# Kernel optimization log

Measured on AMD Instinct MI355X. Metric: run time of the kernel, lower is better.

The kernel has to match this reference:

```python
import jax, jax.numpy as jnp
import numpy as np

EPS_IN = 1e-4   # added to concatenated inputs before variance (as in original)
EPS_OUT = 1e-6  # added after NaN masking (as in original)


def _mdl_masked(a, b):
    """Diagonal-covariance Mahalanobis distance matrix [B,B], NaN-masked, +eps.

    Original TF code builds diag(var), inverts it with tf.linalg.inv and does two
    dense matmuls; mathematically that is an elementwise divide by the per-feature
    variance followed by diff @ diff^T, which is what we compute here.
    """
    in_co = jnp.concatenate((a, b), axis=0) + EPS_IN          # [2B, D]
    var = jnp.var(in_co, axis=0)                              # [D] per-feature variance
    diff = a - b                                              # [B, D]
    q = jnp.einsum('id,jd->ij', diff / var, diff)             # [B, B] = diff @ inv(diag(var)) @ diff^T
    # sqrt of negative entries is NaN in the original; multiply_no_nan zeroes them.
    neg = q < 0.0
    mdist = jnp.where(neg, 0.0, jnp.sqrt(jnp.where(neg, 1.0, q)))
    return mdist + EPS_OUT


def setup_inputs() -> dict:
    key = jax.random.key(0)
    k1, k2, k3 = jax.random.split(key, 3)
    B, D = 8192, 64
    return {
        'anchor': jax.random.normal(k1, (B, D), dtype=jnp.float32),
        'positive': jax.random.normal(k2, (B, D), dtype=jnp.float32),
        'negative': jax.random.normal(k3, (B, D), dtype=jnp.float32),
    }


def reference(anchor, positive, negative):
    ap = _mdl_masked(anchor, positive)   # [B, B]
    an = _mdl_masked(anchor, negative)   # [B, B]
    ap_dis = jnp.sum(ap, axis=-1)        # [B]
    ap_neg = jnp.sum(an, axis=-1)        # [B]
    return (ap_dis, ap_neg)
```

## Files before the change

kernel.cpp:

```cpp
#include <hip/hip_runtime.h>
#include <hip/hip_bf16.h>


typedef short bf16x8 __attribute__((ext_vector_type(8)));
typedef unsigned short u16x8 __attribute__((ext_vector_type(8)));
typedef float f32x4 __attribute__((ext_vector_type(4)));

#define BROWS 8192
#define DFEAT 64
#define NCO   16384
#define EPS_IN  1e-4f
#define EPS_OUT 1e-6f

#define WS_EHL_F 512
#define EHL_PAIR_USHORTS ((size_t)BROWS * 128)

static __device__ inline unsigned short f2bf_rne(float x) {
  unsigned u = __float_as_uint(x);
  unsigned r = (u + 0x7FFF + ((u >> 16) & 1)) >> 16;
  return (unsigned short)r;
}
static __device__ inline float bf2f(unsigned short s) {
  return __uint_as_float(((unsigned)s) << 16);
}

__global__ __launch_bounds__(256) void stats_kernel(
    const float* __restrict__ a, const float* __restrict__ p,
    const float* __restrict__ n, float* __restrict__ stats) {
  __shared__ float acc[6][64];
  int tid = threadIdx.x;
  for (int v = tid; v < 384; v += 256) acc[v >> 6][v & 63] = 0.f;
  __syncthreads();
  const float4* A4 = (const float4*)a;
  const float4* P4 = (const float4*)p;
  const float4* N4 = (const float4*)n;
  size_t base = (size_t)blockIdx.x * 512 + tid;
  float s[3][4] = {}, q[3][4] = {};
  #pragma unroll
  for (int k = 0; k < 2; ++k) {
    size_t idx = base + k * 256;
    float4 va = A4[idx], vp = P4[idx], vn = N4[idx];
    float ea[4] = {va.x, va.y, va.z, va.w};
    float ep[4] = {vp.x, vp.y, vp.z, vp.w};
    float en[4] = {vn.x, vn.y, vn.z, vn.w};
    #pragma unroll
    for (int f = 0; f < 4; ++f) {
      float x0 = ea[f] + EPS_IN; s[0][f] += x0; q[0][f] += x0 * x0;
      float x1 = ep[f] + EPS_IN; s[1][f] += x1; q[1][f] += x1 * x1;
      float x2 = en[f] + EPS_IN; s[2][f] += x2; q[2][f] += x2 * x2;
    }
  }
  #pragma unroll
  for (int g = 0; g < 3; ++g)
    #pragma unroll
    for (int f = 0; f < 4; ++f) {
      float vs = s[g][f], vq = q[g][f];
      vs += __shfl_xor(vs, 16); vs += __shfl_xor(vs, 32);
      vq += __shfl_xor(vq, 16); vq += __shfl_xor(vq, 32);
      s[g][f] = vs; q[g][f] = vq;
    }
  int lane = tid & 63;
  if (lane < 16) {
    int d0 = lane * 4;
    #pragma unroll
    for (int g = 0; g < 3; ++g)
      #pragma unroll
      for (int f = 0; f < 4; ++f) {
        atomicAdd(&acc[2 * g][d0 + f], s[g][f]);
        atomicAdd(&acc[2 * g + 1][d0 + f], q[g][f]);
      }
  }
  __syncthreads();
  for (int v = tid; v < 384; v += 256)
    atomicAdd(&stats[v], acc[v >> 6][v & 63]);
}

__global__ __launch_bounds__(256) void prep_kernel(
    const float* __restrict__ a, const float* __restrict__ p,
    const float* __restrict__ n, const float* __restrict__ stats,
    unsigned short* __restrict__ EHL, float* __restrict__ out) {
  __shared__ float is_s[64];
  int pair = blockIdx.x >> 8;
  int tb   = blockIdx.x & 255;
  int tid  = threadIdx.x;
  if (tid < 32) out[blockIdx.x * 32 + tid] = 8192.0f * EPS_OUT;
  if (tid < 64) {
    float sa = stats[tid], qa = stats[64 + tid];
    float sb = pair ? stats[256 + tid] : stats[128 + tid];
    float qb = pair ? stats[320 + tid] : stats[192 + tid];
    const float invN = 1.0f / (float)NCO;
    float m = (sa + sb) * invN;
    float v = (qa + qb) * invN - m * m;
    is_s[tid] = 1.0f / sqrtf(v);
  }
  __syncthreads();
  const float* bptr = pair ? n : p;
  unsigned short* dst = EHL + (size_t)pair * EHL_PAIR_USHORTS;
  int c0 = tid & 7;
  int rl = tid >> 3;
  int row = tb * 32 + rl;
  int d0 = c0 * 8;
  const float* ar = a    + (size_t)row * DFEAT + d0;
  const float* br = bptr + (size_t)row * DFEAT + d0;
  float4 a0 = *(const float4*)(ar);
  float4 a1 = *(const float4*)(ar + 4);
  float4 b0 = *(const float4*)(br);
  float4 b1 = *(const float4*)(br + 4);
  float e[8] = {a0.x - b0.x, a0.y - b0.y, a0.z - b0.z, a0.w - b0.w,
                a1.x - b1.x, a1.y - b1.y, a1.z - b1.z, a1.w - b1.w};
  u16x8 vh, vl;
  #pragma unroll
  for (int j = 0; j < 8; ++j) {
    float ej = e[j] * is_s[d0 + j];
    unsigned short hi = f2bf_rne(ej);
    vh[j] = hi;
    vl[j] = f2bf_rne(ej - bf2f(hi));
  }
  int cs = c0 ^ (row & 7);
  char* drow = (char*)dst + (size_t)row * 256;
  *(u16x8*)(drow + cs * 16)       = vh;
  *(u16x8*)(drow + (8 + cs) * 16) = vl;
}

#define GLOAD(gsrc, ldst)                                                  \
  __builtin_amdgcn_global_load_lds(                                        \
      (const __attribute__((address_space(1))) void*)(gsrc),               \
      (__attribute__((address_space(3))) void*)(ldst), 16, 0, 0)

__global__ __launch_bounds__(256, 2) void mdist_mfma(
    const unsigned short* __restrict__ EHL, float* __restrict__ out) {
  __shared__ __align__(16) unsigned char sA[32768];
  __shared__ __align__(16) unsigned char sB0[16384];
  __shared__ __align__(16) unsigned char sB1[16384];
  int bid = blockIdx.x;
  int sw  = (bid & 7) * 64 + (bid >> 3);
  int pair  = sw >> 8;
  int ib    = (sw >> 2) & 63;
  int half  = (sw >> 1) & 1;
  int squad = sw & 1;
  const char* base = (const char*)(EHL + (size_t)pair * EHL_PAIR_USHORTS);
  const char* gA = base + (size_t)ib * 32768;
  int tid = threadIdx.x;
  int s0   = half + 2 * squad;
  int smax = (ib < 32) ? 32 : 31;
  int nT   = ((smax - s0) / 4 + 1) * 2;

  {
    const char* gB0 = base + (size_t)(((ib + s0) & 63)) * 32768;
    #pragma unroll
    for (int r = 0; r < 8; ++r) {
      int off = r * 4096 + tid * 16;
      GLOAD(gA + off, sA + off);
    }
    #pragma unroll
    for (int r = 0; r < 4; ++r) {
      int off = r * 4096 + tid * 16;
      GLOAD(gB0 + off, sB0 + off);
    }
  }
  __syncthreads();

  int lane = tid & 63, w = tid >> 6;
  int wr = w >> 1, wc = w & 1;
  int l15 = lane & 15, lg = lane >> 4;

  bf16x8 af[4][4];
  #pragma unroll
  for (int hk = 0; hk < 4; ++hk) {
    int c = ((hk >> 1) << 3) | ((hk & 1) << 2) | lg;
    #pragma unroll
    for (int m = 0; m < 4; ++m) {
      int r = wr * 64 + m * 16 + l15;
      int cs = c ^ (r & 7);
      af[hk][m] = *(const bf16x8*)(sA + r * 256 + cs * 16);
    }
  }

  float rs[4][4];
  #pragma unroll
  for (int m = 0; m < 4; ++m)
    #pragma unroll
    for (int r = 0; r < 4; ++r) rs[m][r] = 0.f;

  const f32x4 zacc = {0.f, 0.f, 0.f, 0.f};
  const int AH[3] = {0, 0, 1};
  const int BH[3] = {0, 1, 0};

  for (int t = 0; t < nT; ++t) {
    unsigned char* wbuf = (t & 1) ? sB0 : sB1;
    const unsigned char* rbuf = (t & 1) ? sB1 : sB0;
    int s   = s0 + 4 * (t >> 1);
    int sub = t & 1;
    if (t + 1 < nT) {
      int tn = t + 1;
      int sn = s0 + 4 * (tn >> 1);
      const char* gs = base + (size_t)((ib + sn) & 63) * 32768 + (tn & 1) * 16384;
      #pragma unroll
      for (int r = 0; r < 4; ++r) {
        int off = r * 4096 + tid * 16;
        GLOAD(gs + off, wbuf + off);
      }
    }
    bf16x8 bf[4][2];
    #pragma unroll
    for (int hk = 0; hk < 4; ++hk) {
      int c = ((hk >> 1) << 3) | ((hk & 1) << 2) | lg;
      #pragma unroll
      for (int nn = 0; nn < 2; ++nn) {
        int r = wc * 32 + nn * 16 + l15;
        int cs = c ^ (r & 7);
        bf[hk][nn] = *(const bf16x8*)(rbuf + r * 256 + cs * 16);
      }
    }
    f32x4 acc[4][2];
    #pragma unroll
    for (int tt = 0; tt < 3; ++tt) {
      #pragma unroll
      for (int ks = 0; ks < 2; ++ks) {
        int ahk = (AH[tt] << 1) | ks;
        int bhk = (BH[tt] << 1) | ks;
        #pragma unroll
        for (int m = 0; m < 4; ++m) {
          #pragma unroll
          for (int nn = 0; nn < 2; ++nn)
            acc[m][nn] = __builtin_amdgcn_mfma_f32_16x16x32_bf16(
                af[ahk][m], bf[bhk][nn],
                (tt == 0 && ks == 0) ? zacc : acc[m][nn], 0, 0, 0);
        }
      }
    }
    if (s == 0) {
      #pragma unroll
      for (int m = 0; m < 4; ++m)
        #pragma unroll
        for (int nn = 0; nn < 2; ++nn)
          #pragma unroll
          for (int r = 0; r < 4; ++r)
            rs[m][r] += __builtin_amdgcn_sqrtf(fmaxf(acc[m][nn][r], 0.f));
    } else {
      float cq0 = 0.f, cq1 = 0.f;
      #pragma unroll
      for (int m = 0; m < 4; ++m)
        #pragma unroll
        for (int nn = 0; nn < 2; ++nn)
          #pragma unroll
          for (int r = 0; r < 4; ++r) {
            float f = __builtin_amdgcn_sqrtf(fmaxf(acc[m][nn][r], 0.f));
            rs[m][r] += f;
            if (nn == 0) cq0 += f; else cq1 += f;
          }
      cq0 += __shfl_xor(cq0, 16); cq0 += __shfl_xor(cq0, 32);
      cq1 += __shfl_xor(cq1, 16); cq1 += __shfl_xor(cq1, 32);
      if (lane < 16) {
        int jb = (ib + s) & 63;
        float* orow = &out[pair * BROWS + jb * 128 + sub * 64 + wc * 32 + l15];
        atomicAdd(orow, cq0);
        atomicAdd(orow + 16, cq1);
      }
    }
    __syncthreads();
  }

  #pragma unroll
  for (int m = 0; m < 4; ++m)
    #pragma unroll
    for (int r = 0; r < 4; ++r) {
      float v = rs[m][r];
      v += __shfl_xor(v, 1);
      v += __shfl_xor(v, 2);
      v += __shfl_xor(v, 4);
      v += __shfl_xor(v, 8);
      rs[m][r] = v;
    }
  if (l15 == 0) {
    int i0 = ib * 128 + wr * 64;
    #pragma unroll
    for (int m = 0; m < 4; ++m)
      #pragma unroll
      for (int r = 0; r < 4; ++r)
        atomicAdd(&out[pair * BROWS + i0 + m * 16 + lg * 4 + r], rs[m][r]);
  }
}

extern "C" void kernel_launch(void* const* d_in, const int* in_sizes, int n_in,
                              void* d_out, int out_size, void* d_ws, size_t ws_size,
                              hipStream_t stream) {
  const float* anchor   = (const float*)d_in[0];
  const float* positive = (const float*)d_in[1];
  const float* negative = (const float*)d_in[2];
  float* out = (float*)d_out;
  float* ws  = (float*)d_ws;

  float* stats = ws;
  unsigned short* EHL = (unsigned short*)(ws + WS_EHL_F);

  hipMemsetAsync(stats, 0, 384 * sizeof(float), stream);
  stats_kernel<<<256, 256, 0, stream>>>(anchor, positive, negative, stats);
  prep_kernel<<<512, 256, 0, stream>>>(anchor, positive, negative, stats, EHL, out);
  mdist_mfma<<<512, 256, 0, stream>>>(EHL, out);
}
```

Baseline: 106.2 us.

## Triple-buffer B tiles by reusing the A LDS buffer, prefetching two tiles ahead

Once the A fragments sit in registers, the sA LDS region is recycled as a third B staging buffer. This lets global_load_lds prefetch run two tiles ahead instead of one. The __syncthreads is replaced with explicit s_waitcnt vmcnt/lgkmcnt plus s_barrier, so each barrier waits only for the stage it needs and more global-load latency can hide behind MFMA work. The fixed vmcnt(10) assumes a steady count of outstanding loads and atomics. Near the end of the loop, or on the s==0 iteration with no atomics, it may release the barrier before the current tile's loads have landed.

```diff
diff --git a/kernel.cpp b/kernel.cpp
--- a/kernel.cpp
+++ b/kernel.cpp
@@ -127,6 +127,15 @@
       (const __attribute__((address_space(1))) void*)(gsrc),               \
       (__attribute__((address_space(3))) void*)(ldst), 16, 0, 0)
 
+#define STAGE4(gs, ld)                                                     \
+  do {                                                                     \
+    _Pragma("unroll")                                                      \
+    for (int r_ = 0; r_ < 4; ++r_) {                                       \
+      int off_ = r_ * 4096 + tid * 16;                                     \
+      GLOAD((gs) + off_, (ld) + off_);                                     \
+    }                                                                      \
+  } while (0)
+
 __global__ __launch_bounds__(256, 2) void mdist_mfma(
     const unsigned short* __restrict__ EHL, float* __restrict__ out) {
   __shared__ __align__(16) unsigned char sA[32768];
@@ -145,20 +154,23 @@
   int smax = (ib < 32) ? 32 : 31;
   int nT   = ((smax - s0) / 4 + 1) * 2;
 
-  {
-    const char* gB0 = base + (size_t)(((ib + s0) & 63)) * 32768;
-    #pragma unroll
-    for (int r = 0; r < 8; ++r) {
-      int off = r * 4096 + tid * 16;
-      GLOAD(gA + off, sA + off);
-    }
-    #pragma unroll
-    for (int r = 0; r < 4; ++r) {
-      int off = r * 4096 + tid * 16;
-      GLOAD(gB0 + off, sB0 + off);
-    }
-  }
-  __syncthreads();
+  auto gsrc = [&](int u) -> const char* {
+    int s_  = s0 + 4 * (u >> 1);
+    int jb_ = (ib + s_) & 63;
+    return base + (size_t)jb_ * 32768 + (size_t)(u & 1) * 16384;
+  };
+
+  #pragma unroll
+  for (int r = 0; r < 8; ++r) {
+    int off = r * 4096 + tid * 16;
+    GLOAD(gA + off, sA + off);
+  }
+  STAGE4(gsrc(0), sB0);
+  STAGE4(gsrc(1), sB1);
+  asm volatile("s_waitcnt vmcnt(4)" ::: "memory");
+  __builtin_amdgcn_sched_barrier(0);
+  __builtin_amdgcn_s_barrier();
+  __builtin_amdgcn_sched_barrier(0);
 
   int lane = tid & 63, w = tid >> 6;
   int wr = w >> 1, wc = w & 1;
@@ -175,6 +187,11 @@
       af[hk][m] = *(const bf16x8*)(sA + r * 256 + cs * 16);
     }
   }
+  asm volatile("s_waitcnt lgkmcnt(0)" ::: "memory");
+  __builtin_amdgcn_sched_barrier(0);
+  __builtin_amdgcn_s_barrier();
+  __builtin_amdgcn_sched_barrier(0);
+  STAGE4(gsrc(2), sA);
 
   float rs[4][4];
   #pragma unroll
@@ -186,21 +203,19 @@
   const int AH[3] = {0, 0, 1};
   const int BH[3] = {0, 1, 0};
 
+  unsigned char* r0 = sB0;
+  unsigned char* r1 = sB1;
+  unsigned char* r2 = sA;
+
   for (int t = 0; t < nT; ++t) {
-    unsigned char* wbuf = (t & 1) ? sB0 : sB1;
-    const unsigned char* rbuf = (t & 1) ? sB1 : sB0;
+    asm volatile("s_waitcnt vmcnt(10)" ::: "memory");
+    __builtin_amdgcn_sched_barrier(0);
+    __builtin_amdgcn_s_barrier();
+    __builtin_amdgcn_sched_barrier(0);
+
     int s   = s0 + 4 * (t >> 1);
     int sub = t & 1;
-    if (t + 1 < nT) {
-      int tn = t + 1;
-      int sn = s0 + 4 * (tn >> 1);
-      const char* gs = base + (size_t)((ib + sn) & 63) * 32768 + (tn & 1) * 16384;
-      #pragma unroll
-      for (int r = 0; r < 4; ++r) {
-        int off = r * 4096 + tid * 16;
-        GLOAD(gs + off, wbuf + off);
-      }
-    }
+
     bf16x8 bf[4][2];
     #pragma unroll
     for (int hk = 0; hk < 4; ++hk) {
@@ -209,7 +224,7 @@
       for (int nn = 0; nn < 2; ++nn) {
         int r = wc * 32 + nn * 16 + l15;
         int cs = c ^ (r & 7);
-        bf[hk][nn] = *(const bf16x8*)(rbuf + r * 256 + cs * 16);
+        bf[hk][nn] = *(const bf16x8*)(r0 + r * 256 + cs * 16);
       }
     }
     f32x4 acc[4][2];
@@ -229,6 +244,13 @@
         }
       }
     }
+
+    asm volatile("s_waitcnt lgkmcnt(0)" ::: "memory");
+    __builtin_amdgcn_sched_barrier(0);
+    __builtin_amdgcn_s_barrier();
+    __builtin_amdgcn_sched_barrier(0);
+    if (t + 3 < nT) STAGE4(gsrc(t + 3), r0);
+
     if (s == 0) {
       #pragma unroll
       for (int m = 0; m < 4; ++m)
@@ -258,7 +280,8 @@
         atomicAdd(orow + 16, cq1);
       }
     }
-    __syncthreads();
+
+    unsigned char* tmp = r0; r0 = r1; r1 = r2; r2 = tmp;
   }
 
   #pragma unroll
```

New measurement: 106.1 us. About the same (-0.1%).

## Drop memset via per-block stat partials and double mdist grid occupancy

Applied to the files above, without the earlier changes.

The stats kernel now writes per-block partial sums to a workspace, and the prep kernel reduces them. This removes the memset launch and the global atomics. The main GEMM kernel reuses one 32KB LDS buffer for the A tile (held in registers afterward) and the B double buffer, which lets four blocks fit per CU instead of two. It also splits work over 1024 blocks with 8-way striding, giving more parallelism but adding an extra sync and more output atomics.

```diff
diff --git a/kernel.cpp b/kernel.cpp
--- a/kernel.cpp
+++ b/kernel.cpp
@@ -11,8 +11,9 @@
 #define NCO   16384
 #define EPS_IN  1e-4f
 #define EPS_OUT 1e-6f
-
-#define WS_EHL_F 512
+#define NPART 64
+
+#define WS_EHL_F  24576
 #define EHL_PAIR_USHORTS ((size_t)BROWS * 128)
 
 static __device__ inline unsigned short f2bf_rne(float x) {
@@ -24,20 +25,26 @@
   return __uint_as_float(((unsigned)s) << 16);
 }
 
+#define GLOAD(gsrc, ldst)                                                  \
+  __builtin_amdgcn_global_load_lds(                                        \
+      (const __attribute__((address_space(1))) void*)(gsrc),               \
+      (__attribute__((address_space(3))) void*)(ldst), 16, 0, 0)
+
 __global__ __launch_bounds__(256) void stats_kernel(
     const float* __restrict__ a, const float* __restrict__ p,
-    const float* __restrict__ n, float* __restrict__ stats) {
-  __shared__ float acc[6][64];
+    const float* __restrict__ n, float* __restrict__ part) {
+  __shared__ float acc[384];
   int tid = threadIdx.x;
-  for (int v = tid; v < 384; v += 256) acc[v >> 6][v & 63] = 0.f;
+  int bid = blockIdx.x;
+  for (int v = tid; v < 384; v += 256) acc[v] = 0.f;
   __syncthreads();
   const float4* A4 = (const float4*)a;
   const float4* P4 = (const float4*)p;
   const float4* N4 = (const float4*)n;
-  size_t base = (size_t)blockIdx.x * 512 + tid;
+  size_t base = (size_t)bid * 2048 + tid;
   float s[3][4] = {}, q[3][4] = {};
   #pragma unroll
-  for (int k = 0; k < 2; ++k) {
+  for (int k = 0; k < 8; ++k) {
     size_t idx = base + k * 256;
     float4 va = A4[idx], vp = P4[idx], vn = N4[idx];
     float ea[4] = {va.x, va.y, va.z, va.w};
@@ -66,28 +73,40 @@
     for (int g = 0; g < 3; ++g)
       #pragma unroll
       for (int f = 0; f < 4; ++f) {
-        atomicAdd(&acc[2 * g][d0 + f], s[g][f]);
-        atomicAdd(&acc[2 * g + 1][d0 + f], q[g][f]);
+        atomicAdd(&acc[(2 * g) * 64 + d0 + f], s[g][f]);
+        atomicAdd(&acc[(2 * g + 1) * 64 + d0 + f], q[g][f]);
       }
   }
   __syncthreads();
   for (int v = tid; v < 384; v += 256)
-    atomicAdd(&stats[v], acc[v >> 6][v & 63]);
+    part[(size_t)bid * 384 + v] = acc[v];
 }
 
 __global__ __launch_bounds__(256) void prep_kernel(
     const float* __restrict__ a, const float* __restrict__ p,
-    const float* __restrict__ n, const float* __restrict__ stats,
+    const float* __restrict__ n, const float* __restrict__ part,
     unsigned short* __restrict__ EHL, float* __restrict__ out) {
+  __shared__ float stats_s[384];
   __shared__ float is_s[64];
   int pair = blockIdx.x >> 8;
   int tb   = blockIdx.x & 255;
   int tid  = threadIdx.x;
   if (tid < 32) out[blockIdx.x * 32 + tid] = 8192.0f * EPS_OUT;
+  {
+    float s1 = 0.f, s2 = 0.f;
+    for (int b = 0; b < NPART; ++b) {
+      const float* pb = part + (size_t)b * 384;
+      s1 += pb[tid];
+      if (tid < 128) s2 += pb[256 + tid];
+    }
+    stats_s[tid] = s1;
+    if (tid < 128) stats_s[256 + tid] = s2;
+  }
+  __syncthreads();
   if (tid < 64) {
-    float sa = stats[tid], qa = stats[64 + tid];
-    float sb = pair ? stats[256 + tid] : stats[128 + tid];
-    float qb = pair ? stats[320 + tid] : stats[192 + tid];
+    float sa = stats_s[tid], qa = stats_s[64 + tid];
+    float sb = pair ? stats_s[256 + tid] : stats_s[128 + tid];
+    float qb = pair ? stats_s[320 + tid] : stats_s[192 + tid];
     const float invN = 1.0f / (float)NCO;
     float m = (sa + sb) * invN;
     float v = (qa + qb) * invN - m * m;
@@ -122,41 +141,26 @@
   *(u16x8*)(drow + (8 + cs) * 16) = vl;
 }
 
-#define GLOAD(gsrc, ldst)                                                  \
-  __builtin_amdgcn_global_load_lds(                                        \
-      (const __attribute__((address_space(1))) void*)(gsrc),               \
-      (__attribute__((address_space(3))) void*)(ldst), 16, 0, 0)
-
-__global__ __launch_bounds__(256, 2) void mdist_mfma(
+__global__ __launch_bounds__(256, 4) void mdist_mfma(
     const unsigned short* __restrict__ EHL, float* __restrict__ out) {
-  __shared__ __align__(16) unsigned char sA[32768];
-  __shared__ __align__(16) unsigned char sB0[16384];
-  __shared__ __align__(16) unsigned char sB1[16384];
+  __shared__ __align__(16) unsigned char smem[32768];
+  unsigned char* sB0 = smem;
+  unsigned char* sB1 = smem + 16384;
   int bid = blockIdx.x;
-  int sw  = (bid & 7) * 64 + (bid >> 3);
-  int pair  = sw >> 8;
-  int ib    = (sw >> 2) & 63;
-  int half  = (sw >> 1) & 1;
-  int squad = sw & 1;
+  int sw  = (bid & 7) * 128 + (bid >> 3);
+  int pair = sw >> 9;
+  int ib   = (sw >> 3) & 63;
+  int r0   = sw & 7;
   const char* base = (const char*)(EHL + (size_t)pair * EHL_PAIR_USHORTS);
   const char* gA = base + (size_t)ib * 32768;
   int tid = threadIdx.x;
-  int s0   = half + 2 * squad;
   int smax = (ib < 32) ? 32 : 31;
-  int nT   = ((smax - s0) / 4 + 1) * 2;
-
-  {
-    const char* gB0 = base + (size_t)(((ib + s0) & 63)) * 32768;
-    #pragma unroll
-    for (int r = 0; r < 8; ++r) {
-      int off = r * 4096 + tid * 16;
-      GLOAD(gA + off, sA + off);
-    }
-    #pragma unroll
-    for (int r = 0; r < 4; ++r) {
-      int off = r * 4096 + tid * 16;
-      GLOAD(gB0 + off, sB0 + off);
-    }
+  int nT   = ((smax - r0) / 8 + 1) * 2;
+
+  #pragma unroll
+  for (int rr = 0; rr < 8; ++rr) {
+    int off = rr * 4096 + tid * 16;
+    GLOAD(gA + off, smem + off);
   }
   __syncthreads();
 
@@ -170,17 +174,28 @@
     int c = ((hk >> 1) << 3) | ((hk & 1) << 2) | lg;
     #pragma unroll
     for (int m = 0; m < 4; ++m) {
-      int r = wr * 64 + m * 16 + l15;
-      int cs = c ^ (r & 7);
-      af[hk][m] = *(const bf16x8*)(sA + r * 256 + cs * 16);
-    }
-  }
+      int rr = wr * 64 + m * 16 + l15;
+      int cs = c ^ (rr & 7);
+      af[hk][m] = *(const bf16x8*)(smem + rr * 256 + cs * 16);
+    }
+  }
+  __syncthreads();
+
+  {
+    const char* gB0 = base + (size_t)((ib + r0) & 63) * 32768;
+    #pragma unroll
+    for (int rr = 0; rr < 4; ++rr) {
+      int off = rr * 4096 + tid * 16;
+      GLOAD(gB0 + off, sB0 + off);
+    }
+  }
+  __syncthreads();
 
   float rs[4][4];
   #pragma unroll
   for (int m = 0; m < 4; ++m)
     #pragma unroll
-    for (int r = 0; r < 4; ++r) rs[m][r] = 0.f;
+    for (int rr = 0; rr < 4; ++rr) rs[m][rr] = 0.f;
 
   const f32x4 zacc = {0.f, 0.f, 0.f, 0.f};
   const int AH[3] = {0, 0, 1};
@@ -189,15 +204,15 @@
   for (int t = 0; t < nT; ++t) {
     unsigned char* wbuf = (t & 1) ? sB0 : sB1;
     const unsigned char* rbuf = (t & 1) ? sB1 : sB0;
-    int s   = s0 + 4 * (t >> 1);
+    int s   = r0 + 8 * (t >> 1);
     int sub = t & 1;
     if (t + 1 < nT) {
       int tn = t + 1;
-      int sn = s0 + 4 * (tn >> 1);
+      int sn = r0 + 8 * (tn >> 1);
       const char* gs = base + (size_t)((ib + sn) & 63) * 32768 + (tn & 1) * 16384;
       #pragma unroll
-      for (int r = 0; r < 4; ++r) {
-        int off = r * 4096 + tid * 16;
+      for (int rr = 0; rr < 4; ++rr) {
+        int off = rr * 4096 + tid * 16;
         GLOAD(gs + off, wbuf + off);
       }
     }
@@ -207,9 +222,9 @@
       int c = ((hk >> 1) << 3) | ((hk & 1) << 2) | lg;
       #pragma unroll
       for (int nn = 0; nn < 2; ++nn) {
-        int r = wc * 32 + nn * 16 + l15;
-        int cs = c ^ (r & 7);
-        bf[hk][nn] = *(const bf16x8*)(rbuf + r * 256 + cs * 16);
+        int rr = wc * 32 + nn * 16 + l15;
+        int cs = c ^ (rr & 7);
+        bf[hk][nn] = *(const bf16x8*)(rbuf + rr * 256 + cs * 16);
       }
     }
     f32x4 acc[4][2];
@@ -235,8 +250,8 @@
         #pragma unroll
         for (int nn = 0; nn < 2; ++nn)
           #pragma unroll
-          for (int r = 0; r < 4; ++r)
-            rs[m][r] += __builtin_amdgcn_sqrtf(fmaxf(acc[m][nn][r], 0.f));
+          for (int rr = 0; rr < 4; ++rr)
+            rs[m][rr] += __builtin_amdgcn_sqrtf(fmaxf(acc[m][nn][rr], 0.f));
     } else {
       float cq0 = 0.f, cq1 = 0.f;
       #pragma unroll
@@ -244,9 +259,9 @@
         #pragma unroll
         for (int nn = 0; nn < 2; ++nn)
           #pragma unroll
-          for (int r = 0; r < 4; ++r) {
-            float f = __builtin_amdgcn_sqrtf(fmaxf(acc[m][nn][r], 0.f));
-            rs[m][r] += f;
+          for (int rr = 0; rr < 4; ++rr) {
+            float f = __builtin_amdgcn_sqrtf(fmaxf(acc[m][nn][rr], 0.f));
+            rs[m][rr] += f;
             if (nn == 0) cq0 += f; else cq1 += f;
           }
       cq0 += __shfl_xor(cq0, 16); cq0 += __shfl_xor(cq0, 32);
@@ -264,21 +279,21 @@
   #pragma unroll
   for (int m = 0; m < 4; ++m)
     #pragma unroll
-    for (int r = 0; r < 4; ++r) {
-      float v = rs[m][r];
+    for (int rr = 0; rr < 4; ++rr) {
+      float v = rs[m][rr];
       v += __shfl_xor(v, 1);
       v += __shfl_xor(v, 2);
       v += __shfl_xor(v, 4);
       v += __shfl_xor(v, 8);
-      rs[m][r] = v;
+      rs[m][rr] = v;
     }
   if (l15 == 0) {
     int i0 = ib * 128 + wr * 64;
     #pragma unroll
     for (int m = 0; m < 4; ++m)
       #pragma unroll
-      for (int r = 0; r < 4; ++r)
-        atomicAdd(&out[pair * BROWS + i0 + m * 16 + lg * 4 + r], rs[m][r]);
+      for (int rr = 0; rr < 4; ++rr)
+        atomicAdd(&out[pair * BROWS + i0 + m * 16 + lg * 4 + rr], rs[m][rr]);
   }
 }
 
@@ -291,11 +306,10 @@
   float* out = (float*)d_out;
   float* ws  = (float*)d_ws;
 
-  float* stats = ws;
+  float* part = ws;
   unsigned short* EHL = (unsigned short*)(ws + WS_EHL_F);
 
-  hipMemsetAsync(stats, 0, 384 * sizeof(float), stream);
-  stats_kernel<<<256, 256, 0, stream>>>(anchor, positive, negative, stats);
-  prep_kernel<<<512, 256, 0, stream>>>(anchor, positive, negative, stats, EHL, out);
-  mdist_mfma<<<512, 256, 0, stream>>>(EHL, out);
-}
+  stats_kernel<<<64, 256, 0, stream>>>(anchor, positive, negative, part);
+  prep_kernel<<<512, 256, 0, stream>>>(anchor, positive, negative, part, EHL, out);
+  mdist_mfma<<<1024, 256, 0, stream>>>(EHL, out);
+}
```

After: 177.1 us. 66.8% more time.
